# Kernel optimization log

Measured on AMD Instinct MI355X. Metric: run time of the kernel, lower is better.

The kernel has to match this reference:

```python
import jax, jax.numpy as jnp
import numpy as np

R, S, D_IN, WIDTH, K = 8192, 128, 16, 64, 8  # rays, samples/ray, feat dim, net_width, net_kernels


def setup_inputs() -> dict:
    key = jax.random.key(0)
    ks = jax.random.split(key, 8)
    he = jax.nn.initializers.he_uniform()
    idxs = jax.random.randint(ks[0], (R, S), 0, K, dtype=jnp.int32)
    xs = jax.random.normal(ks[1], (R, S, D_IN), dtype=jnp.float32)
    # MultiMLP params: net_depth=2 hidden MultiDense layers + 1 output layer, each with K kernels
    W0 = he(ks[2], (K, D_IN, WIDTH), jnp.float32)
    b0 = jnp.zeros((K, WIDTH), jnp.float32)
    W1 = he(ks[3], (K, WIDTH, WIDTH), jnp.float32)
    b1 = jnp.zeros((K, WIDTH), jnp.float32)
    W2 = he(ks[4], (K, WIDTH, 1), jnp.float32)
    b2 = jnp.zeros((K, 1), jnp.float32)
    return {"idxs": idxs, "xs": xs, "W0": W0, "b0": b0, "W1": W1, "b1": b1, "W2": W2, "b2": b2}


def _multi_dense(idx, x, W, b):
    """Per-sample kernel select: out[n] = x[n] @ W[idx[n]] + b[idx[n]].

    x: [N, d], W: [K, d, f], b: [K, f], idx: [N] int. Loop is over the small
    fixed kernel count K (not a data dim); avoids materializing an [N, d, f]
    gathered-weight tensor.
    """
    out = jnp.zeros((x.shape[0], W.shape[-1]), x.dtype)
    zero = jnp.zeros((), x.dtype)
    for k in range(W.shape[0]):
        sel = (idx == k)[:, None]
        out = out + jnp.where(sel, x @ W[k] + b[k], zero)
    return out


def reference(idxs, xs, W0, b0, W1, b1, W2, b2):
    batch_shape = idxs.shape  # (R, S)
    idx = idxs.reshape(-1)
    h = xs.reshape(-1, xs.shape[-1])
    h = jax.nn.relu(_multi_dense(idx, h, W0, b0))
    h = jax.nn.relu(_multi_dense(idx, h, W1, b1))
    out = _multi_dense(idx, h, W2, b2)  # [N, 1] density
    return out.reshape(*batch_shape, 1)
```

## Files before the change

### kernel.cpp

```cpp
#include <hip/hip_runtime.h>


typedef __attribute__((ext_vector_type(8))) short bfrag;
typedef __attribute__((ext_vector_type(4))) float ffrag;

#define SPAN        512
#define NSPANS      2048
#define IMG_STRIDE  15360
#define WS_NEED     ((size_t)(8 * IMG_STRIDE))

__device__ __forceinline__ unsigned short bf16r(float f) {
    unsigned int u = __float_as_uint(f);
    u += 0x7fffu + ((u >> 16) & 1u);
    return (unsigned short)(u >> 16);
}
__device__ __forceinline__ unsigned int pack_trunc(float hiF, float loF) {
    return __builtin_amdgcn_perm(__float_as_uint(hiF), __float_as_uint(loF), 0x07060302u);
}
__device__ __forceinline__ unsigned int cvtpk(float lo, float hi) {
    unsigned int r;
    asm("v_cvt_pk_bf16_f32 %0, %1, %2" : "=v"(r) : "v"(lo), "v"(hi));
    return r;
}
__device__ __forceinline__ bfrag mkfrag(unsigned int a, unsigned int b,
                                        unsigned int c, unsigned int d) {
    union { unsigned int u[4]; bfrag f; } x;
    x.u[0] = a; x.u[1] = b; x.u[2] = c; x.u[3] = d;
    return x.f;
}

__global__ void k_build_images(const float* __restrict__ W0, const float* __restrict__ b0,
                               const float* __restrict__ W1, const float* __restrict__ b1,
                               const float* __restrict__ W2, const float* __restrict__ b2,
                               unsigned char* __restrict__ wsB) {
    const int k = blockIdx.x >> 3, p = blockIdx.x & 7, t = threadIdx.x;
    unsigned char* img = wsB + k * IMG_STRIDE;
    unsigned short* w0a = (unsigned short*)img;
    unsigned short* w1a = (unsigned short*)(img + 4096);
    unsigned short* w2a = (unsigned short*)(img + 12288);
    float* bias = (float*)(img + 14336);
    {
        int e = p * 256 + t;
        int j = e & 7, lane = (e >> 3) & 63, nt = e >> 9, q = lane >> 4, l15 = lane & 15;
        unsigned short v = 0;
        if (q < 2) {
            v = bf16r(W0[k * 1024 + (q * 8 + j) * 64 + nt * 16 + l15]);
        } else if (q == 2 && j < 2) {
            float b = b0[k * 64 + nt * 16 + l15];
            unsigned short hb = bf16r(b);
            if (j == 0) v = hb;
            else        v = bf16r(b - __uint_as_float((unsigned int)hb << 16));
        }
        w0a[e] = v;
    }
    #pragma unroll
    for (int i = 0; i < 2; ++i) {
        int e = p * 512 + i * 256 + t;
        int j = e & 7, lane = (e >> 3) & 63, s = (e >> 9) & 1, nt = e >> 10;
        int q = lane >> 4, l15 = lane & 15;
        int h = s * 32 + ((j < 4) ? (q * 4 + j) : (16 + q * 4 + (j - 4)));
        w1a[e] = bf16r(W1[k * 4096 + h * 64 + nt * 16 + l15]);
    }
    if (t < 128) {
        int e = p * 128 + t;
        int j = e & 7, lane = (e >> 3) & 63, s = e >> 9, q = lane >> 4, l15 = lane & 15;
        int h = s * 32 + ((j < 4) ? (q * 4 + j) : (16 + q * 4 + (j - 4)));
        w2a[e] = (l15 == 0) ? bf16r(W2[k * 64 + h]) : (unsigned short)0;
    }
    if (p == 0) {
        if (t < 64) bias[t] = b1[k * 64 + t];
        else if (t == 64) bias[64] = b2[k];
    }
}

__global__ __launch_bounds__(256, 2) void k_fused(const int* __restrict__ idxs,
                                                  const float* __restrict__ xs,
                                                  const unsigned char* __restrict__ wsB,
                                                  float* __restrict__ out) {
    __shared__ int wcnt[2][4][8];
    __shared__ int bsbase[2][4][8];
    __shared__ int cntS[8], startS[8];
    __shared__ unsigned short sId[SPAN];
    __shared__ __align__(16) unsigned short Xg[SPAN * 16];
    __shared__ float outBuf[SPAN];

    const int tid = threadIdx.x, lane = tid & 63, w = tid >> 6;
    const int q = lane >> 4, l15 = lane & 15;
    const int base = blockIdx.x * SPAN;

    int kreg[2], lrank[2];
    #pragma unroll
    for (int it = 0; it < 2; ++it) {
        int k = idxs[base + it * 256 + tid];
        kreg[it] = k;
        unsigned long long mymask = 0;
        #pragma unroll
        for (int kk = 0; kk < 8; ++kk) {
            unsigned long long m = __ballot(k == kk);
            if (k == kk) mymask = m;
            if (lane == 0) wcnt[it][w][kk] = (int)__popcll(m);
        }
        lrank[it] = (int)__popcll(mymask & ((1ull << lane) - 1ull));
    }
    __syncthreads();
    if (tid < 8) {
        int c = 0;
        for (int it = 0; it < 2; ++it)
            for (int w2 = 0; w2 < 4; ++w2) c += wcnt[it][w2][tid];
        cntS[tid] = c;
    }
    __syncthreads();
    if (tid == 0) {
        int s = 0;
        for (int k = 0; k < 8; ++k) { startS[k] = s; s += cntS[k]; }
    }
    __syncthreads();
    if (tid < 64) {
        int it = tid >> 5, w2 = (tid >> 3) & 3, kk = tid & 7;
        int b = startS[kk];
        for (int it2 = 0; it2 < it; ++it2)
            for (int w3 = 0; w3 < 4; ++w3) b += wcnt[it2][w3][kk];
        for (int w3 = 0; w3 < w2; ++w3) b += wcnt[it][w3][kk];
        bsbase[it][w2][kk] = b;
    }
    __syncthreads();
    #pragma unroll
    for (int it = 0; it < 2; ++it)
        sId[bsbase[it][w][kreg[it]] + lrank[it]] = (unsigned short)(it * 256 + tid);
    __syncthreads();

    #pragma unroll
    for (int it = 0; it < 2; ++it) {
        const int r = it * 256 + tid;
        const int gid = base + (int)sId[r];
        const float4* p = (const float4*)(xs + (size_t)gid * 16);
        float4 f0 = p[0], f1 = p[1], f2 = p[2], f3 = p[3];
        uint4 lo, hi;
        lo.x = pack_trunc(f0.y, f0.x); lo.y = pack_trunc(f0.w, f0.z);
        lo.z = pack_trunc(f1.y, f1.x); lo.w = pack_trunc(f1.w, f1.z);
        hi.x = pack_trunc(f2.y, f2.x); hi.y = pack_trunc(f2.w, f2.z);
        hi.z = pack_trunc(f3.y, f3.x); hi.w = pack_trunc(f3.w, f3.z);
        const int g = r >> 4, m = r & 15;
        *(uint4*)(Xg + g * 256 + m * 8)       = lo;
        *(uint4*)(Xg + g * 256 + 128 + m * 8) = hi;
    }
    __syncthreads();

    #pragma unroll
    for (int kk2 = 0; kk2 < 2; ++kk2) {
        const int k = w + kk2 * 4;
        const int cnt = cntS[k];
        if (cnt == 0) continue;
        const int start = startS[k];
        const unsigned char* img = wsB + k * IMG_STRIDE;

        bfrag w0f[4], w1f[4][2], w2f[2];
        #pragma unroll
        for (int nt = 0; nt < 4; ++nt)
            w0f[nt] = *(const bfrag*)(img + nt * 1024 + lane * 16);
        #pragma unroll
        for (int nt = 0; nt < 4; ++nt)
            #pragma unroll
            for (int s = 0; s < 2; ++s)
                w1f[nt][s] = *(const bfrag*)(img + 4096 + ((nt * 2 + s) * 64 + lane) * 16);
        #pragma unroll
        for (int s = 0; s < 2; ++s)
            w2f[s] = *(const bfrag*)(img + 12288 + (s * 64 + lane) * 16);
        const float* bias = (const float*)(img + 14336);
        ffrag b1v[4];
        #pragma unroll
        for (int nt = 0; nt < 4; ++nt)
            b1v[nt] = *(const ffrag*)(bias + nt * 16 + q * 4);
        ffrag c2 = {0.f, 0.f, 0.f, 0.f};
        if (q == 0) c2[0] = bias[64];

        const int nst = (cnt + 15) >> 4;

        auto loadB = [&](int st) -> bfrag {
            int r = start + st * 16 + l15;
            int rm = start + cnt - 1;
            r = r < rm ? r : rm;
            bfrag bv = *(const bfrag*)(Xg + (r >> 4) * 256 + (q & 1) * 128 + (r & 15) * 8);
            if (q == 2) { bv[0] = (short)0x3F80; bv[1] = (short)0x3F80; }
            return bv;
        };

        auto chain = [&](bfrag bv) -> ffrag {
            ffrag acc0[4];
            #pragma unroll
            for (int nt = 0; nt < 4; ++nt) {
                ffrag z = {0.f, 0.f, 0.f, 0.f};
                acc0[nt] = __builtin_amdgcn_mfma_f32_16x16x32_bf16(w0f[nt], bv, z, 0, 0, 0);
            }
            unsigned int P[8];
            #pragma unroll
            for (int nt = 0; nt < 4; ++nt) {
                float v0 = acc0[nt][0] > 0.f ? acc0[nt][0] : 0.f;
                float v1 = acc0[nt][1] > 0.f ? acc0[nt][1] : 0.f;
                float v2 = acc0[nt][2] > 0.f ? acc0[nt][2] : 0.f;
                float v3 = acc0[nt][3] > 0.f ? acc0[nt][3] : 0.f;
                P[nt * 2]     = cvtpk(v0, v1);
                P[nt * 2 + 1] = cvtpk(v2, v3);
            }
            bfrag h10 = mkfrag(P[0], P[1], P[2], P[3]);
            bfrag h11 = mkfrag(P[4], P[5], P[6], P[7]);
            ffrag acc1[4];
            #pragma unroll
            for (int nt = 0; nt < 4; ++nt) {
                acc1[nt] = __builtin_amdgcn_mfma_f32_16x16x32_bf16(w1f[nt][0], h10, b1v[nt], 0, 0, 0);
                acc1[nt] = __builtin_amdgcn_mfma_f32_16x16x32_bf16(w1f[nt][1], h11, acc1[nt], 0, 0, 0);
            }
            unsigned int Qp[8];
            #pragma unroll
            for (int nt = 0; nt < 4; ++nt) {
                float v0 = acc1[nt][0] > 0.f ? acc1[nt][0] : 0.f;
                float v1 = acc1[nt][1] > 0.f ? acc1[nt][1] : 0.f;
                float v2 = acc1[nt][2] > 0.f ? acc1[nt][2] : 0.f;
                float v3 = acc1[nt][3] > 0.f ? acc1[nt][3] : 0.f;
                Qp[nt * 2]     = cvtpk(v0, v1);
                Qp[nt * 2 + 1] = cvtpk(v2, v3);
            }
            bfrag h20 = mkfrag(Qp[0], Qp[1], Qp[2], Qp[3]);
            bfrag h21 = mkfrag(Qp[4], Qp[5], Qp[6], Qp[7]);
            ffrag d = __builtin_amdgcn_mfma_f32_16x16x32_bf16(w2f[0], h20, c2, 0, 0, 0);
            d = __builtin_amdgcn_mfma_f32_16x16x32_bf16(w2f[1], h21, d, 0, 0, 0);
            return d;
        };

        int st = 0;
        bfrag bA = loadB(0);
        bfrag bB = loadB(1);
        for (; st + 1 < nst; st += 2) {
            bfrag pA = loadB(st + 2);
            bfrag pB = loadB(st + 3);
            ffrag dA = chain(bA);
            ffrag dB = chain(bB);
            if (q == 0) {
                int rowA = st * 16 + l15;
                if (rowA < cnt) outBuf[sId[start + rowA]] = dA[0];
                int rowB = (st + 1) * 16 + l15;
                if (rowB < cnt) outBuf[sId[start + rowB]] = dB[0];
            }
            bA = pA; bB = pB;
        }
        if (st < nst) {
            ffrag dA = chain(bA);
            if (q == 0) {
                int row = st * 16 + l15;
                if (row < cnt) outBuf[sId[start + row]] = dA[0];
            }
        }
    }
    __syncthreads();

    ((float2*)(out + base))[tid] = ((const float2*)outBuf)[tid];
}

__global__ void k_fallback(const int* __restrict__ idxs, const float* __restrict__ xs,
                           const float* __restrict__ W0, const float* __restrict__ b0,
                           const float* __restrict__ W1, const float* __restrict__ b1,
                           const float* __restrict__ W2, const float* __restrict__ b2,
                           float* __restrict__ out, int N) {
    int n = blockIdx.x * blockDim.x + threadIdx.x;
    if (n >= N) return;
    int k = idxs[n];
    float h0[64];
    #pragma unroll
    for (int j = 0; j < 64; ++j) h0[j] = b0[k * 64 + j];
    for (int i = 0; i < 16; ++i) {
        float xi = xs[(size_t)n * 16 + i];
        #pragma unroll
        for (int j = 0; j < 64; ++j) h0[j] = fmaf(xi, W0[k * 1024 + i * 64 + j], h0[j]);
    }
    #pragma unroll
    for (int j = 0; j < 64; ++j) h0[j] = fmaxf(h0[j], 0.f);
    float acc = b2[k];
    for (int jc = 0; jc < 4; ++jc) {
        float h1[16];
        #pragma unroll
        for (int j = 0; j < 16; ++j) h1[j] = b1[k * 64 + jc * 16 + j];
        for (int i = 0; i < 64; ++i) {
            float hv = h0[i];
            #pragma unroll
            for (int j = 0; j < 16; ++j)
                h1[j] = fmaf(hv, W1[k * 4096 + i * 64 + jc * 16 + j], h1[j]);
        }
        #pragma unroll
        for (int j = 0; j < 16; ++j) acc = fmaf(fmaxf(h1[j], 0.f), W2[k * 64 + jc * 16 + j], acc);
    }
    out[n] = acc;
}

extern "C" void kernel_launch(void* const* d_in, const int* in_sizes, int n_in,
                              void* d_out, int out_size, void* d_ws, size_t ws_size,
                              hipStream_t stream) {
    const int*   idxs = (const int*)d_in[0];
    const float* xs   = (const float*)d_in[1];
    const float* W0   = (const float*)d_in[2];
    const float* b0   = (const float*)d_in[3];
    const float* W1   = (const float*)d_in[4];
    const float* b1   = (const float*)d_in[5];
    const float* W2   = (const float*)d_in[6];
    const float* b2   = (const float*)d_in[7];
    float* out = (float*)d_out;
    const int N = in_sizes[0];

    if (N != SPAN * NSPANS || ws_size < WS_NEED) {
        k_fallback<<<(N + 255) / 256, 256, 0, stream>>>(idxs, xs, W0, b0, W1, b1, W2, b2, out, N);
        return;
    }

    unsigned char* wsB = (unsigned char*)d_ws;
    k_build_images<<<64, 256, 0, stream>>>(W0, b0, W1, b1, W2, b2, wsB);
    k_fused<<<NSPANS, 256, 0, stream>>>(idxs, xs, wsB, out);
}
```

Baseline: 127.0 us.

## Double span per block and split every kernel's tiles across all four waves

Each block now handles 1024 samples instead of 512, using four index-sorting iterations, and launches half as many blocks. Previously each wave owned two fixed kernel groups. Now all eight kernel groups are walked by every wave, and a group's 16-row tiles are interleaved across the four waves. This is meant to balance work across waves when group sizes differ and to amortize weight loads over larger groups. In exchange, each wave loads weights for all eight kernels, the software prefetch of the next tiles is dropped, and LDS use doubles, which may limit occupancy.

Measured after the change: 136.9 us. +7.8%, slower.

```diff
diff --git a/kernel.cpp b/kernel.cpp
--- a/kernel.cpp
+++ b/kernel.cpp
@@ -4,8 +4,9 @@
 typedef __attribute__((ext_vector_type(8))) short bfrag;
 typedef __attribute__((ext_vector_type(4))) float ffrag;
 
-#define SPAN        512
-#define NSPANS      2048
+#define SPAN        1024
+#define NSPANS      1024
+#define SITER       4
 #define IMG_STRIDE  15360
 #define WS_NEED     ((size_t)(8 * IMG_STRIDE))
 
@@ -77,20 +78,20 @@
                                                   const float* __restrict__ xs,
                                                   const unsigned char* __restrict__ wsB,
                                                   float* __restrict__ out) {
-    __shared__ int wcnt[2][4][8];
-    __shared__ int bsbase[2][4][8];
+    __shared__ int wcnt[SITER][4][8];
+    __shared__ int bsbase[SITER][4][8];
     __shared__ int cntS[8], startS[8];
     __shared__ unsigned short sId[SPAN];
     __shared__ __align__(16) unsigned short Xg[SPAN * 16];
-    __shared__ float outBuf[SPAN];
+    __shared__ __align__(16) float outBuf[SPAN];
 
     const int tid = threadIdx.x, lane = tid & 63, w = tid >> 6;
     const int q = lane >> 4, l15 = lane & 15;
     const int base = blockIdx.x * SPAN;
 
-    int kreg[2], lrank[2];
-    #pragma unroll
-    for (int it = 0; it < 2; ++it) {
+    int kreg[SITER], lrank[SITER];
+    #pragma unroll
+    for (int it = 0; it < SITER; ++it) {
         int k = idxs[base + it * 256 + tid];
         kreg[it] = k;
         unsigned long long mymask = 0;
@@ -105,7 +106,7 @@
     __syncthreads();
     if (tid < 8) {
         int c = 0;
-        for (int it = 0; it < 2; ++it)
+        for (int it = 0; it < SITER; ++it)
             for (int w2 = 0; w2 < 4; ++w2) c += wcnt[it][w2][tid];
         cntS[tid] = c;
     }
@@ -115,7 +116,7 @@
         for (int k = 0; k < 8; ++k) { startS[k] = s; s += cntS[k]; }
     }
     __syncthreads();
-    if (tid < 64) {
+    if (tid < 32 * SITER) {
         int it = tid >> 5, w2 = (tid >> 3) & 3, kk = tid & 7;
         int b = startS[kk];
         for (int it2 = 0; it2 < it; ++it2)
@@ -125,12 +126,12 @@
     }
     __syncthreads();
     #pragma unroll
-    for (int it = 0; it < 2; ++it)
+    for (int it = 0; it < SITER; ++it)
         sId[bsbase[it][w][kreg[it]] + lrank[it]] = (unsigned short)(it * 256 + tid);
     __syncthreads();
 
     #pragma unroll
-    for (int it = 0; it < 2; ++it) {
+    for (int it = 0; it < SITER; ++it) {
         const int r = it * 256 + tid;
         const int gid = base + (int)sId[r];
         const float4* p = (const float4*)(xs + (size_t)gid * 16);
@@ -146,9 +147,7 @@
     }
     __syncthreads();
 
-    #pragma unroll
-    for (int kk2 = 0; kk2 < 2; ++kk2) {
-        const int k = w + kk2 * 4;
+    for (int k = 0; k < 8; ++k) {
         const int cnt = cntS[k];
         if (cnt == 0) continue;
         const int start = startS[k];
@@ -227,33 +226,31 @@
             return d;
         };
 
-        int st = 0;
-        bfrag bA = loadB(0);
-        bfrag bB = loadB(1);
-        for (; st + 1 < nst; st += 2) {
-            bfrag pA = loadB(st + 2);
-            bfrag pB = loadB(st + 3);
-            ffrag dA = chain(bA);
-            ffrag dB = chain(bB);
-            if (q == 0) {
-                int rowA = st * 16 + l15;
-                if (rowA < cnt) outBuf[sId[start + rowA]] = dA[0];
-                int rowB = (st + 1) * 16 + l15;
-                if (rowB < cnt) outBuf[sId[start + rowB]] = dB[0];
-            }
-            bA = pA; bB = pB;
+        for (int stA = w; stA < nst; stA += 8) {
+            const int stB = stA + 4;
+            bfrag bA = loadB(stA);
+            if (stB < nst) {
+                bfrag bB = loadB(stB);
+                ffrag dA = chain(bA);
+                ffrag dB = chain(bB);
+                if (q == 0) {
+                    int rowA = stA * 16 + l15;
+                    if (rowA < cnt) outBuf[sId[start + rowA]] = dA[0];
+                    int rowB = stB * 16 + l15;
+                    if (rowB < cnt) outBuf[sId[start + rowB]] = dB[0];
+                }
+            } else {
+                ffrag dA = chain(bA);
+                if (q == 0) {
+                    int row = stA * 16 + l15;
+                    if (row < cnt) outBuf[sId[start + row]] = dA[0];
+                }
+            }
         }
-        if (st < nst) {
-            ffrag dA = chain(bA);
-            if (q == 0) {
-                int row = st * 16 + l15;
-                if (row < cnt) outBuf[sId[start + row]] = dA[0];
-            }
-        }
-    }
-    __syncthreads();
-
-    ((float2*)(out + base))[tid] = ((const float2*)outBuf)[tid];
+    }
+    __syncthreads();
+
+    ((float4*)(out + base))[tid] = ((const float4*)outBuf)[tid];
 }
 
 __global__ void k_fallback(const int* __restrict__ idxs, const float* __restrict__ xs,
```
